# Performance work log

Measured on AMD Instinct MI355X. Metric: run time of the kernel, lower is better.

## Reference

```python
import jax, jax.numpy as jnp
import numpy as np
import math

BATCH, CLS, ATT_DIM, IMG_DIM = 256, 500, 1024, 1024
ATT_HC, HIDDEN_C = 256, 1024
T_TEMP = 10.0
DEGREE = 30
THRESH = math.cos(math.pi * DEGREE / 180.0)
NEG = -9.0e15


def setup_inputs() -> dict:
    key = jax.random.key(0)
    ks = jax.random.split(key, 9)
    inp = {
        "image_feats": jax.random.normal(ks[0], (BATCH, IMG_DIM), dtype=jnp.float32),
        "attributes": jax.random.normal(ks[1], (CLS, ATT_DIM), dtype=jnp.float32),
        "unused": 0,
        # learned parameters (kaiming-like scaling)
        "att_g": jax.random.normal(ks[2], (ATT_DIM, ATT_HC), dtype=jnp.float32) / math.sqrt(ATT_DIM),
        "img_w": jax.random.normal(ks[3], (IMG_DIM, HIDDEN_C), dtype=jnp.float32) / math.sqrt(IMG_DIM),
        "sem_w": jax.random.normal(ks[4], (ATT_DIM, HIDDEN_C), dtype=jnp.float32) / math.sqrt(ATT_DIM),
        "sem_b": jax.random.normal(ks[5], (1, HIDDEN_C), dtype=jnp.float32) / math.sqrt(IMG_DIM),
        "fc_w": jax.random.normal(ks[6], (1, HIDDEN_C), dtype=jnp.float32) / math.sqrt(HIDDEN_C),
        "fc_b": jax.random.normal(ks[7], (1,), dtype=jnp.float32) / math.sqrt(HIDDEN_C),
    }
    return inp


def _get_new_attribute(attributes, att_g):
    # project attributes, cosine similarity between all class pairs
    g = attributes @ att_g                                    # [cls, att_hC]
    gn = g / jnp.linalg.norm(g, axis=1, keepdims=True)        # row-normalize
    sim = gn @ gn.T                                           # [cls, cls] cosine sims
    raw = jnp.where(sim > THRESH, sim, NEG)                   # angular-threshold mask
    attention = jax.nn.softmax(raw * T_TEMP, axis=1)          # [cls, cls]
    return attention @ attributes                             # [cls, att_dim]


def reference(image_feats, attributes, unused, att_g, img_w, sem_w, sem_b, fc_w, fc_b):
    att_outs = _get_new_attribute(attributes, att_g)          # [cls, att_dim]
    # factor the broadcast: identical math to matmul on expanded tensors
    img_h = image_feats @ img_w                               # [batch, hidden]
    sem_h = att_outs @ sem_w                                  # [cls, hidden]
    hidden = jax.nn.relu(img_h[:, None, :] + sem_h[None, :, :] + sem_b[None, :, :])  # [batch, cls, hidden]
    out = jnp.einsum('bch,h->bc', hidden, fc_w[0]) + fc_b[0]  # [batch, cls]
    return out
```

## Files before the change

kernel.cpp:

```cpp
#include <hip/hip_runtime.h>
#include <math.h>

#define BATCH 256
#define CLS 500
#define T_TEMP_ 10.0f
#define THRESH_ 0.86602540378443864676f
#define NEGV -9.0e15f

typedef __attribute__((ext_vector_type(8))) short short8;
typedef __attribute__((ext_vector_type(8))) unsigned short u16x8;
typedef __attribute__((ext_vector_type(4))) unsigned short u16x4;
typedef __attribute__((ext_vector_type(4))) float f32x4;
typedef __attribute__((ext_vector_type(2))) float f32x2;

static __device__ __forceinline__ unsigned short f2bf(float x) {
    unsigned int u = __builtin_bit_cast(unsigned int, x);
    u += 0x7fff + ((u >> 16) & 1);
    return (unsigned short)(u >> 16);
}
static __device__ __forceinline__ float bf2f(unsigned short v) {
    return __builtin_bit_cast(float, (unsigned int)v << 16);
}
static __device__ __forceinline__ float fel(const float4& v, int j) { return (&v.x)[j]; }
static __device__ __forceinline__ u16x8 pack8(const float4& a, const float4& b) {
    u16x8 o;
    o[0] = f2bf(a.x); o[1] = f2bf(a.y); o[2] = f2bf(a.z); o[3] = f2bf(a.w);
    o[4] = f2bf(b.x); o[5] = f2bf(b.y); o[6] = f2bf(b.z); o[7] = f2bf(b.w);
    return o;
}

__global__ __launch_bounds__(256) void mega_gemm(
    const float* __restrict__ attrs, const float* __restrict__ attg,
    const float* __restrict__ imgf, const float* __restrict__ imgw,
    const float* __restrict__ semw,
    float* __restrict__ gpart, unsigned short* __restrict__ imgP,
    unsigned short* __restrict__ asemP)
{
    __shared__ unsigned short As[64][40];
    __shared__ unsigned short Bs[128][40];
    const int t = threadIdx.x;
    const int bid = blockIdx.x;

    const int w = t >> 6, lane = t & 63;
    const int wr = w >> 1, wc = w & 1;
    const int fr = lane & 15, kg = lane >> 4;
    const int as_row = t >> 2, as_kq = t & 3;
    const int bs_nc = (t & 31) * 4, bs_kr = t >> 5;

    const float* A; const float* Bf;
    int ar0, alim, n0, k0, klen, bstride, split;
    if (bid < 128) {
        const int mt = bid >> 4, nt = (bid >> 3) & 1; split = bid & 7;
        A = attrs; alim = CLS; ar0 = mt * 64;
        Bf = attg; bstride = 256; n0 = nt * 128;
        k0 = split * 128; klen = 128;
    } else if (bid < 192) {
        const int idx = bid - 128; split = idx & 1;
        const int nt = (idx >> 1) & 7, mt = idx >> 4;
        A = imgf; alim = 256; ar0 = mt * 64;
        Bf = imgw; bstride = 1024; n0 = nt * 128;
        k0 = split * 512; klen = 512;
    } else {
        const int idx = bid - 192; split = idx & 1;
        const int nt = (idx >> 1) & 7, mt = idx >> 4;
        A = attrs; alim = CLS; ar0 = mt * 64;
        Bf = semw; bstride = 1024; n0 = nt * 128;
        k0 = split * 512; klen = 512;
    }

    f32x4 acc[2][4];
    #pragma unroll
    for (int i = 0; i < 2; ++i)
        #pragma unroll
        for (int j = 0; j < 4; ++j) acc[i][j] = (f32x4){0.f, 0.f, 0.f, 0.f};

    for (int kb = k0; kb < k0 + klen; kb += 32) {
        {
            const int gr = ar0 + as_row;
            float4 v0 = make_float4(0.f,0.f,0.f,0.f), v1 = v0;
            if (gr < alim) {
                const float* ap = &A[(size_t)gr * 1024 + kb + as_kq * 8];
                v0 = *(const float4*)ap; v1 = *(const float4*)(ap + 4);
            }
            *(u16x8*)&As[as_row][as_kq * 8] = pack8(v0, v1);
        }
        {
            const float* bp = &Bf[(size_t)(kb + bs_kr * 4) * bstride + n0 + bs_nc];
            float4 r0 = *(const float4*)(bp);
            float4 r1 = *(const float4*)(bp + bstride);
            float4 r2 = *(const float4*)(bp + 2 * bstride);
            float4 r3 = *(const float4*)(bp + 3 * bstride);
            #pragma unroll
            for (int j = 0; j < 4; ++j) {
                unsigned int lo = (unsigned int)f2bf(fel(r0, j)) | ((unsigned int)f2bf(fel(r1, j)) << 16);
                unsigned int hi = (unsigned int)f2bf(fel(r2, j)) | ((unsigned int)f2bf(fel(r3, j)) << 16);
                uint2 u2; u2.x = lo; u2.y = hi;
                *(uint2*)&Bs[bs_nc + j][bs_kr * 4] = u2;
            }
        }
        __syncthreads();
        short8 af[2], bfr[4];
        #pragma unroll
        for (int i = 0; i < 2; ++i) af[i] = *(short8*)&As[wr * 32 + i * 16 + fr][kg * 8];
        #pragma unroll
        for (int j = 0; j < 4; ++j) bfr[j] = *(short8*)&Bs[wc * 64 + j * 16 + fr][kg * 8];
        #pragma unroll
        for (int i = 0; i < 2; ++i)
            #pragma unroll
            for (int j = 0; j < 4; ++j)
                acc[i][j] = __builtin_amdgcn_mfma_f32_16x16x32_bf16(af[i], bfr[j], acc[i][j], 0, 0, 0);
        __syncthreads();
    }

    const int orow0 = ar0 + wr * 32, ocol0 = n0 + wc * 64;
    if (bid < 128) {
        float* Gp = gpart + (size_t)split * (512 * 256);
        #pragma unroll
        for (int i = 0; i < 2; ++i) {
            const int r0 = orow0 + i * 16 + kg * 4;
            #pragma unroll
            for (int j = 0; j < 4; ++j) {
                const int cc = ocol0 + j * 16 + fr;
                #pragma unroll
                for (int r = 0; r < 4; ++r)
                    Gp[(size_t)(r0 + r) * 256 + cc] = acc[i][j][r];
            }
        }
    } else {
        unsigned short* Cw = (bid < 192)
            ? imgP  + (size_t)split * (256 * 1024)
            : asemP + (size_t)split * (512 * 1024);
        #pragma unroll
        for (int i = 0; i < 2; ++i) {
            const int r0 = orow0 + i * 16 + kg * 4;
            #pragma unroll
            for (int j = 0; j < 4; ++j) {
                const int cc = ocol0 + j * 16 + fr;
                #pragma unroll
                for (int r = 0; r < 4; ++r)
                    Cw[(size_t)(r0 + r) * 1024 + cc] = f2bf(acc[i][j][r]);
            }
        }
    }
}

__global__ __launch_bounds__(256) void reduce_norm_kernel(
    const float* __restrict__ part, unsigned short* __restrict__ gn_bf)
{
    const int c = blockIdx.x, t = threadIdx.x;
    float v = 0.f;
    #pragma unroll
    for (int z = 0; z < 8; ++z) v += part[(size_t)z * (512 * 256) + c * 256 + t];
    float ss = v * v;
    #pragma unroll
    for (int off = 32; off >= 1; off >>= 1) ss += __shfl_down(ss, off);
    __shared__ float red[4];
    const int wave = t >> 6, lane = t & 63;
    if (lane == 0) red[wave] = ss;
    __syncthreads();
    const float tot = red[0] + red[1] + red[2] + red[3];
    const float rn  = 1.f / sqrtf(tot);
    gn_bf[c * 256 + t] = f2bf(v * rn);
}

__global__ __launch_bounds__(256) void sim_kernel(
    const unsigned short* __restrict__ gn, float* __restrict__ S)
{
    __shared__ unsigned short As[64][40];
    __shared__ unsigned short Bs[128][40];
    const int t  = threadIdx.x;
    const int ar0 = blockIdx.x * 64;
    const int n0  = blockIdx.y * 128;

    const int w = t >> 6, lane = t & 63;
    const int wr = w >> 1, wc = w & 1;
    const int fr = lane & 15, kg = lane >> 4;
    const int a_row = t >> 2, a_k = (t & 3) * 8;
    const int b_row = t >> 1, b_k = (t & 1) * 16;
    const int gra = ar0 + a_row;
    const int grb = n0 + b_row;
    const bool va = gra < CLS;
    const bool vb = grb < CLS;
    const size_t abase = (size_t)gra * 256 + a_k;
    const size_t bbase = (size_t)grb * 256 + b_k;

    u16x8 zz = {0,0,0,0,0,0,0,0};
    u16x8 pa = zz, pb0 = zz, pb1 = zz;
    if (va) pa = *(const u16x8*)&gn[abase];
    if (vb) { pb0 = *(const u16x8*)&gn[bbase]; pb1 = *(const u16x8*)&gn[bbase + 8]; }

    f32x4 acc[2][4];
    #pragma unroll
    for (int i = 0; i < 2; ++i)
        #pragma unroll
        for (int j = 0; j < 4; ++j) acc[i][j] = (f32x4){0.f, 0.f, 0.f, 0.f};

    for (int kb = 0; kb < 256; kb += 32) {
        *(u16x8*)&As[a_row][a_k] = pa;
        *(u16x8*)&Bs[b_row][b_k] = pb0;
        *(u16x8*)&Bs[b_row][b_k + 8] = pb1;
        __syncthreads();

        const int kn = kb + 32;
        if (kn < 256) {
            if (va) pa = *(const u16x8*)&gn[abase + kn];
            if (vb) { pb0 = *(const u16x8*)&gn[bbase + kn]; pb1 = *(const u16x8*)&gn[bbase + kn + 8]; }
        }

        short8 af[2], bfr[4];
        #pragma unroll
        for (int i = 0; i < 2; ++i) af[i] = *(short8*)&As[wr * 32 + i * 16 + fr][kg * 8];
        #pragma unroll
        for (int j = 0; j < 4; ++j) bfr[j] = *(short8*)&Bs[wc * 64 + j * 16 + fr][kg * 8];
        #pragma unroll
        for (int i = 0; i < 2; ++i)
            #pragma unroll
            for (int j = 0; j < 4; ++j)
                acc[i][j] = __builtin_amdgcn_mfma_f32_16x16x32_bf16(af[i], bfr[j], acc[i][j], 0, 0, 0);
        __syncthreads();
    }

    const int orow0 = ar0 + wr * 32, ocol0 = n0 + wc * 64;
    #pragma unroll
    for (int i = 0; i < 2; ++i) {
        const int r0 = orow0 + i * 16 + kg * 4;
        #pragma unroll
        for (int j = 0; j < 4; ++j) {
            const int cc = ocol0 + j * 16 + fr;
            if (cc >= CLS) continue;
            #pragma unroll
            for (int r = 0; r < 4; ++r) {
                const int rr = r0 + r;
                if (rr < CLS) S[(size_t)rr * CLS + cc] = acc[i][j][r];
            }
        }
    }
}

__global__ __launch_bounds__(256) void softmax_gather_kernel(
    const float* __restrict__ sim, const unsigned short* __restrict__ asemP,
    const float* __restrict__ semb, unsigned short* __restrict__ sem_h)
{
    const int c = blockIdx.x, t = threadIdx.x;
    __shared__ float p_s[512];
    __shared__ float redm[4];
    __shared__ float reds[4];

    const float d0 = sim[(size_t)c * CLS + t];
    const float d1 = (t + 256 < CLS) ? sim[(size_t)c * CLS + t + 256] : NEGV;

    float vmax = fmaxf((d0 > THRESH_) ? d0 : NEGV, (d1 > THRESH_) ? d1 : NEGV);
    #pragma unroll
    for (int off = 32; off >= 1; off >>= 1) vmax = fmaxf(vmax, __shfl_down(vmax, off));
    const int wave = t >> 6, lane = t & 63;
    if (lane == 0) redm[wave] = vmax;
    __syncthreads();
    const float m = fmaxf(fmaxf(redm[0], redm[1]), fmaxf(redm[2], redm[3]));

    const float p0 = (d0 > THRESH_) ? expf(T_TEMP_ * (d0 - m)) : 0.f;
    const float p1 = (d1 > THRESH_) ? expf(T_TEMP_ * (d1 - m)) : 0.f;
    p_s[t] = p0;
    p_s[t + 256] = p1;
    float vsum = p0 + p1;
    #pragma unroll
    for (int off = 32; off >= 1; off >>= 1) vsum += __shfl_down(vsum, off);
    if (lane == 0) reds[wave] = vsum;
    __syncthreads();
    const float inv = 1.f / (reds[0] + reds[1] + reds[2] + reds[3]);

    float acc[4] = {0.f, 0.f, 0.f, 0.f};
    for (int base = 0; base < 512; base += 64) {
        const float pv_l = p_s[base + lane];
        unsigned long long mask = __ballot(pv_l > 0.f);
        while (mask) {
            const int l = __ffsll((long long)mask) - 1;
            mask &= mask - 1;
            const int c2 = base + l;
            const float pv = p_s[c2];
            const unsigned short* a0 = &asemP[(size_t)c2 * 1024 + t];
            const unsigned short* a1 = a0 + (size_t)512 * 1024;
            #pragma unroll
            for (int j = 0; j < 4; ++j)
                acc[j] += pv * (bf2f(a0[256 * j]) + bf2f(a1[256 * j]));
        }
    }
    #pragma unroll
    for (int j = 0; j < 4; ++j)
        sem_h[(size_t)c * 1024 + t + 256 * j] =
            f2bf(acc[j] * inv + semb[t + 256 * j]);
}

__global__ __launch_bounds__(256) void fused_out_partial(
    const unsigned short* __restrict__ imgP, const unsigned short* __restrict__ sem_h,
    const float* __restrict__ fc_w, float* __restrict__ outpart)
{
    __shared__ float imgs[64][36];
    __shared__ float sems[64][36];
    __shared__ float fcs[32];

    const size_t istride = (size_t)256 * 1024;
    const int t  = threadIdx.x;
    const int tb = t >> 4, tc = t & 15;
    const int b0 = blockIdx.x * 64, c0 = blockIdx.y * 64;
    const int h0 = blockIdx.z * 32;

    if (t < 8) *(float4*)&fcs[t * 4] = *(const float4*)&fc_w[h0 + t * 4];

    {
        const int row = t >> 2, col = (t & 3) * 8;
        f32x4 iv0 = {0.f,0.f,0.f,0.f}, iv1 = iv0;
        const unsigned short* pi = &imgP[(size_t)(b0 + row) * 1024 + h0 + col];
        #pragma unroll
        for (int z = 0; z < 2; ++z) {
            u16x8 vz = *(const u16x8*)(pi + (size_t)z * istride);
            iv0[0] += bf2f(vz[0]); iv0[1] += bf2f(vz[1]);
            iv0[2] += bf2f(vz[2]); iv0[3] += bf2f(vz[3]);
            iv1[0] += bf2f(vz[4]); iv1[1] += bf2f(vz[5]);
            iv1[2] += bf2f(vz[6]); iv1[3] += bf2f(vz[7]);
        }
        *(f32x4*)&imgs[row][col]     = iv0;
        *(f32x4*)&imgs[row][col + 4] = iv1;

        f32x4 sv0 = {0.f,0.f,0.f,0.f}, sv1 = sv0;
        if (c0 + row < CLS) {
            u16x8 vz = *(const u16x8*)&sem_h[(size_t)(c0 + row) * 1024 + h0 + col];
            sv0[0] = bf2f(vz[0]); sv0[1] = bf2f(vz[1]);
            sv0[2] = bf2f(vz[2]); sv0[3] = bf2f(vz[3]);
            sv1[0] = bf2f(vz[4]); sv1[1] = bf2f(vz[5]);
            sv1[2] = bf2f(vz[6]); sv1[3] = bf2f(vz[7]);
        }
        *(f32x4*)&sems[row][col]     = sv0;
        *(f32x4*)&sems[row][col + 4] = sv1;
    }
    __syncthreads();

    f32x2 acc2[4][4];
    #pragma unroll
    for (int i = 0; i < 4; ++i)
        #pragma unroll
        for (int j = 0; j < 4; ++j) acc2[i][j] = (f32x2){0.f, 0.f};

    #pragma unroll
    for (int h4 = 0; h4 < 8; ++h4) {
        f32x4 ia[4], sa[4];
        #pragma unroll
        for (int i = 0; i < 4; ++i) ia[i] = *(f32x4*)&imgs[tb + 16 * i][h4 * 4];
        #pragma unroll
        for (int j = 0; j < 4; ++j) sa[j] = *(f32x4*)&sems[tc + 16 * j][h4 * 4];
        const f32x4 wv = *(const f32x4*)&fcs[h4 * 4];
        #pragma unroll
        for (int e2 = 0; e2 < 2; ++e2) {
            const f32x2 w2 = {wv[2 * e2], wv[2 * e2 + 1]};
            f32x2 ia2[4], sa2[4];
            #pragma unroll
            for (int i = 0; i < 4; ++i) ia2[i] = (f32x2){ia[i][2 * e2], ia[i][2 * e2 + 1]};
            #pragma unroll
            for (int j = 0; j < 4; ++j) sa2[j] = (f32x2){sa[j][2 * e2], sa[j][2 * e2 + 1]};
            #pragma unroll
            for (int i = 0; i < 4; ++i)
                #pragma unroll
                for (int j = 0; j < 4; ++j) {
                    f32x2 s = ia2[i] + sa2[j];
                    s = __builtin_elementwise_max(s, (f32x2){0.f, 0.f});
                    acc2[i][j] += s * w2;
                }
        }
    }

    const int nh = blockIdx.z;
    #pragma unroll
    for (int i = 0; i < 4; ++i) {
        const int b = b0 + tb + 16 * i;
        #pragma unroll
        for (int j = 0; j < 4; ++j) {
            const int cc = c0 + tc + 16 * j;
            if (cc < CLS)
                outpart[((size_t)nh * BATCH + b) * CLS + cc] = acc2[i][j][0] + acc2[i][j][1];
        }
    }
}

__global__ __launch_bounds__(256) void finalize_kernel(
    const float* __restrict__ partial, const float* __restrict__ fc_b,
    float* __restrict__ out)
{
    const int idx = blockIdx.x * 256 + threadIdx.x;
    if (idx >= BATCH * CLS) return;
    float s = fc_b[0];
    #pragma unroll
    for (int nh = 0; nh < 32; ++nh)
        s += partial[(size_t)nh * (BATCH * CLS) + idx];
    out[idx] = s;
}

extern "C" void kernel_launch(void* const* d_in, const int* in_sizes, int n_in,
                              void* d_out, int out_size, void* d_ws, size_t ws_size,
                              hipStream_t stream)
{
    const float* imgf  = (const float*)d_in[0];
    const float* attrs = (const float*)d_in[1];
    const float* attg  = (const float*)d_in[3];
    const float* imgw  = (const float*)d_in[4];
    const float* semw  = (const float*)d_in[5];
    const float* semb  = (const float*)d_in[6];
    const float* fcw   = (const float*)d_in[7];
    const float* fcb   = (const float*)d_in[8];
    float* out = (float*)d_out;

    char* ws = (char*)d_ws;
    size_t off = 0;
    auto alloc = [&](size_t b) { size_t o = off; off = (off + b + 255) & ~(size_t)255; return o; };
    float* gpart          = (float*)(ws + alloc((size_t)8 * 512 * 256 * 4));
    unsigned short* gn_bf = (unsigned short*)(ws + alloc((size_t)500 * 256 * 2));
    float* sim            = (float*)(ws + alloc((size_t)CLS * CLS * 4));
    unsigned short* imgP  = (unsigned short*)(ws + alloc((size_t)2 * 256 * 1024 * 2));
    unsigned short* asemP = (unsigned short*)(ws + alloc((size_t)2 * 512 * 1024 * 2));
    unsigned short* sem_h = (unsigned short*)(ws + alloc((size_t)500 * 1024 * 2));
    float* outP           = (float*)(ws + alloc((size_t)32 * BATCH * CLS * 4));

    mega_gemm<<<320, 256, 0, stream>>>(attrs, attg, imgf, imgw, semw,
                                       gpart, imgP, asemP);
    reduce_norm_kernel<<<CLS, 256, 0, stream>>>(gpart, gn_bf);
    sim_kernel<<<dim3(8, 4), 256, 0, stream>>>(gn_bf, sim);
    softmax_gather_kernel<<<CLS, 256, 0, stream>>>(sim, asemP, semb, sem_h);
    fused_out_partial<<<dim3(4, 8, 32), 256, 0, stream>>>(imgP, sem_h, fcw, outP);
    finalize_kernel<<<(BATCH * CLS + 255) / 256, 256, 0, stream>>>(outP, fcb, out);
}
```

Before: 64.44 us.

## Fuse similarity GEMM with softmax and sparse gather into one kernel

Merges the cosine-similarity GEMM and the softmax/gather kernels into a single kernel. Each of 8 blocks computes a 64-row strip of the similarity matrix into LDS, then computes a thresholded softmax per row and records up to 16 nonzero weights with their column indices. It then gathers the weighted attribute projections, falling back to a full scan when a row has more than 16 hits. This removes the global round trip of the similarity matrix and one kernel launch. The cost is that only 8 blocks run, and each block walks its 64 rows one after another, so parallelism is far lower than the previous 500-block gather. The kernel also needs roughly 150 KB of LDS per block.

```diff
diff --git a/kernel.cpp b/kernel.cpp
--- a/kernel.cpp
+++ b/kernel.cpp
@@ -6,6 +6,7 @@
 #define T_TEMP_ 10.0f
 #define THRESH_ 0.86602540378443864676f
 #define NEGV -9.0e15f
+#define CAP 16
 
 typedef __attribute__((ext_vector_type(8))) short short8;
 typedef __attribute__((ext_vector_type(8))) unsigned short u16x8;
@@ -163,131 +164,172 @@
     gn_bf[c * 256 + t] = f2bf(v * rn);
 }
 
-__global__ __launch_bounds__(256) void sim_kernel(
-    const unsigned short* __restrict__ gn, float* __restrict__ S)
-{
+__global__ __launch_bounds__(256) void sim_softmax_gather(
+    const unsigned short* __restrict__ gn, const unsigned short* __restrict__ asemP,
+    const float* __restrict__ semb, unsigned short* __restrict__ sem_h)
+{
+    __shared__ float simS[64][512];
     __shared__ unsigned short As[64][40];
     __shared__ unsigned short Bs[128][40];
-    const int t  = threadIdx.x;
-    const int ar0 = blockIdx.x * 64;
-    const int n0  = blockIdx.y * 128;
-
+    __shared__ int   cnt_s[64];
+    __shared__ int   hitc2[64][CAP];
+    __shared__ float hitw[64][CAP];
+    __shared__ float mrow[64];
+    __shared__ float invrow[64];
+
+    const int t = threadIdx.x;
+    const int r0g = blockIdx.x * 64;
     const int w = t >> 6, lane = t & 63;
     const int wr = w >> 1, wc = w & 1;
     const int fr = lane & 15, kg = lane >> 4;
     const int a_row = t >> 2, a_k = (t & 3) * 8;
     const int b_row = t >> 1, b_k = (t & 1) * 16;
-    const int gra = ar0 + a_row;
-    const int grb = n0 + b_row;
+
+    const int gra = r0g + a_row;
     const bool va = gra < CLS;
-    const bool vb = grb < CLS;
     const size_t abase = (size_t)gra * 256 + a_k;
-    const size_t bbase = (size_t)grb * 256 + b_k;
-
-    u16x8 zz = {0,0,0,0,0,0,0,0};
-    u16x8 pa = zz, pb0 = zz, pb1 = zz;
-    if (va) pa = *(const u16x8*)&gn[abase];
-    if (vb) { pb0 = *(const u16x8*)&gn[bbase]; pb1 = *(const u16x8*)&gn[bbase + 8]; }
-
-    f32x4 acc[2][4];
-    #pragma unroll
-    for (int i = 0; i < 2; ++i)
-        #pragma unroll
-        for (int j = 0; j < 4; ++j) acc[i][j] = (f32x4){0.f, 0.f, 0.f, 0.f};
-
-    for (int kb = 0; kb < 256; kb += 32) {
-        *(u16x8*)&As[a_row][a_k] = pa;
-        *(u16x8*)&Bs[b_row][b_k] = pb0;
-        *(u16x8*)&Bs[b_row][b_k + 8] = pb1;
-        __syncthreads();
-
-        const int kn = kb + 32;
-        if (kn < 256) {
-            if (va) pa = *(const u16x8*)&gn[abase + kn];
-            if (vb) { pb0 = *(const u16x8*)&gn[bbase + kn]; pb1 = *(const u16x8*)&gn[bbase + kn + 8]; }
-        }
-
-        short8 af[2], bfr[4];
-        #pragma unroll
-        for (int i = 0; i < 2; ++i) af[i] = *(short8*)&As[wr * 32 + i * 16 + fr][kg * 8];
-        #pragma unroll
-        for (int j = 0; j < 4; ++j) bfr[j] = *(short8*)&Bs[wc * 64 + j * 16 + fr][kg * 8];
+
+    for (int nt = 0; nt < 4; ++nt) {
+        const int n0 = nt * 128;
+        const int grb = n0 + b_row;
+        const bool vb = grb < CLS;
+        const size_t bbase = (size_t)grb * 256 + b_k;
+
+        u16x8 zz = {0,0,0,0,0,0,0,0};
+        u16x8 pa = zz, pb0 = zz, pb1 = zz;
+        if (va) pa = *(const u16x8*)&gn[abase];
+        if (vb) { pb0 = *(const u16x8*)&gn[bbase]; pb1 = *(const u16x8*)&gn[bbase + 8]; }
+
+        f32x4 acc[2][4];
         #pragma unroll
         for (int i = 0; i < 2; ++i)
             #pragma unroll
-            for (int j = 0; j < 4; ++j)
-                acc[i][j] = __builtin_amdgcn_mfma_f32_16x16x32_bf16(af[i], bfr[j], acc[i][j], 0, 0, 0);
-        __syncthreads();
-    }
-
-    const int orow0 = ar0 + wr * 32, ocol0 = n0 + wc * 64;
-    #pragma unroll
-    for (int i = 0; i < 2; ++i) {
-        const int r0 = orow0 + i * 16 + kg * 4;
-        #pragma unroll
-        for (int j = 0; j < 4; ++j) {
-            const int cc = ocol0 + j * 16 + fr;
-            if (cc >= CLS) continue;
-            #pragma unroll
-            for (int r = 0; r < 4; ++r) {
-                const int rr = r0 + r;
-                if (rr < CLS) S[(size_t)rr * CLS + cc] = acc[i][j][r];
-            }
-        }
-    }
-}
-
-__global__ __launch_bounds__(256) void softmax_gather_kernel(
-    const float* __restrict__ sim, const unsigned short* __restrict__ asemP,
-    const float* __restrict__ semb, unsigned short* __restrict__ sem_h)
-{
-    const int c = blockIdx.x, t = threadIdx.x;
-    __shared__ float p_s[512];
-    __shared__ float redm[4];
-    __shared__ float reds[4];
-
-    const float d0 = sim[(size_t)c * CLS + t];
-    const float d1 = (t + 256 < CLS) ? sim[(size_t)c * CLS + t + 256] : NEGV;
-
-    float vmax = fmaxf((d0 > THRESH_) ? d0 : NEGV, (d1 > THRESH_) ? d1 : NEGV);
-    #pragma unroll
-    for (int off = 32; off >= 1; off >>= 1) vmax = fmaxf(vmax, __shfl_down(vmax, off));
-    const int wave = t >> 6, lane = t & 63;
-    if (lane == 0) redm[wave] = vmax;
+            for (int j = 0; j < 4; ++j) acc[i][j] = (f32x4){0.f, 0.f, 0.f, 0.f};
+
+        for (int kb = 0; kb < 256; kb += 32) {
+            *(u16x8*)&As[a_row][a_k] = pa;
+            *(u16x8*)&Bs[b_row][b_k] = pb0;
+            *(u16x8*)&Bs[b_row][b_k + 8] = pb1;
+            __syncthreads();
+
+            const int kn = kb + 32;
+            if (kn < 256) {
+                if (va) pa = *(const u16x8*)&gn[abase + kn];
+                if (vb) { pb0 = *(const u16x8*)&gn[bbase + kn]; pb1 = *(const u16x8*)&gn[bbase + kn + 8]; }
+            }
+
+            short8 af[2], bfr[4];
+            #pragma unroll
+            for (int i = 0; i < 2; ++i) af[i] = *(short8*)&As[wr * 32 + i * 16 + fr][kg * 8];
+            #pragma unroll
+            for (int j = 0; j < 4; ++j) bfr[j] = *(short8*)&Bs[wc * 64 + j * 16 + fr][kg * 8];
+            #pragma unroll
+            for (int i = 0; i < 2; ++i)
+                #pragma unroll
+                for (int j = 0; j < 4; ++j)
+                    acc[i][j] = __builtin_amdgcn_mfma_f32_16x16x32_bf16(af[i], bfr[j], acc[i][j], 0, 0, 0);
+            __syncthreads();
+        }
+
+        const int orow0 = wr * 32, ocol0 = n0 + wc * 64;
+        #pragma unroll
+        for (int i = 0; i < 2; ++i) {
+            const int r0 = orow0 + i * 16 + kg * 4;
+            #pragma unroll
+            for (int j = 0; j < 4; ++j) {
+                const int cc = ocol0 + j * 16 + fr;
+                #pragma unroll
+                for (int r = 0; r < 4; ++r)
+                    simS[r0 + r][cc] = acc[i][j][r];
+            }
+        }
+    }
     __syncthreads();
-    const float m = fmaxf(fmaxf(redm[0], redm[1]), fmaxf(redm[2], redm[3]));
-
-    const float p0 = (d0 > THRESH_) ? expf(T_TEMP_ * (d0 - m)) : 0.f;
-    const float p1 = (d1 > THRESH_) ? expf(T_TEMP_ * (d1 - m)) : 0.f;
-    p_s[t] = p0;
-    p_s[t + 256] = p1;
-    float vsum = p0 + p1;
-    #pragma unroll
-    for (int off = 32; off >= 1; off >>= 1) vsum += __shfl_down(vsum, off);
-    if (lane == 0) reds[wave] = vsum;
+
+    for (int i = 0; i < 16; ++i) {
+        const int rl = w * 16 + i;
+        const int r  = r0g + rl;
+        float vals[8];
+        float vmax = NEGV;
+        if (r < CLS) {
+            #pragma unroll
+            for (int ch = 0; ch < 8; ++ch) {
+                const int c2 = ch * 64 + lane;
+                const float d = (c2 < CLS) ? simS[rl][c2] : NEGV;
+                vals[ch] = d;
+                vmax = fmaxf(vmax, (d > THRESH_) ? d : NEGV);
+            }
+        } else {
+            #pragma unroll
+            for (int ch = 0; ch < 8; ++ch) vals[ch] = NEGV;
+        }
+        #pragma unroll
+        for (int off = 32; off >= 1; off >>= 1) vmax = fmaxf(vmax, __shfl_down(vmax, off));
+        vmax = __shfl(vmax, 0);
+        float pvs[8];
+        float s = 0.f;
+        #pragma unroll
+        for (int ch = 0; ch < 8; ++ch) {
+            const float pv = (vals[ch] > THRESH_) ? expf(T_TEMP_ * (vals[ch] - vmax)) : 0.f;
+            pvs[ch] = pv; s += pv;
+        }
+        #pragma unroll
+        for (int off = 32; off >= 1; off >>= 1) s += __shfl_down(s, off);
+        s = __shfl(s, 0);
+        const float inv = (r < CLS) ? 1.f / s : 0.f;
+        int count = 0;
+        #pragma unroll
+        for (int ch = 0; ch < 8; ++ch) {
+            unsigned long long mk = __ballot(pvs[ch] > 0.f);
+            while (mk) {
+                const int l = __ffsll((long long)mk) - 1;
+                mk &= mk - 1;
+                const float wgt = __shfl(pvs[ch], l) * inv;
+                if (count < CAP && lane == 0) {
+                    hitc2[rl][count] = ch * 64 + l;
+                    hitw[rl][count]  = wgt;
+                }
+                ++count;
+            }
+        }
+        if (lane == 0) { cnt_s[rl] = count; mrow[rl] = vmax; invrow[rl] = inv; }
+    }
     __syncthreads();
-    const float inv = 1.f / (reds[0] + reds[1] + reds[2] + reds[3]);
-
-    float acc[4] = {0.f, 0.f, 0.f, 0.f};
-    for (int base = 0; base < 512; base += 64) {
-        const float pv_l = p_s[base + lane];
-        unsigned long long mask = __ballot(pv_l > 0.f);
-        while (mask) {
-            const int l = __ffsll((long long)mask) - 1;
-            mask &= mask - 1;
-            const int c2 = base + l;
-            const float pv = p_s[c2];
-            const unsigned short* a0 = &asemP[(size_t)c2 * 1024 + t];
-            const unsigned short* a1 = a0 + (size_t)512 * 1024;
-            #pragma unroll
-            for (int j = 0; j < 4; ++j)
-                acc[j] += pv * (bf2f(a0[256 * j]) + bf2f(a1[256 * j]));
-        }
-    }
-    #pragma unroll
-    for (int j = 0; j < 4; ++j)
-        sem_h[(size_t)c * 1024 + t + 256 * j] =
-            f2bf(acc[j] * inv + semb[t + 256 * j]);
+
+    for (int rl = 0; rl < 64; ++rl) {
+        const int r = r0g + rl;
+        if (r >= CLS) continue;
+        float acc[4] = {0.f, 0.f, 0.f, 0.f};
+        const int n = cnt_s[rl];
+        if (n <= CAP) {
+            for (int k = 0; k < n; ++k) {
+                const int c2 = hitc2[rl][k];
+                const float wgt = hitw[rl][k];
+                const unsigned short* a0 = &asemP[(size_t)c2 * 1024 + t];
+                const unsigned short* a1 = a0 + (size_t)512 * 1024;
+                #pragma unroll
+                for (int j = 0; j < 4; ++j)
+                    acc[j] += wgt * (bf2f(a0[256 * j]) + bf2f(a1[256 * j]));
+            }
+        } else {
+            const float mr = mrow[rl], ir = invrow[rl];
+            for (int c2 = 0; c2 < CLS; ++c2) {
+                const float d = simS[rl][c2];
+                if (d > THRESH_) {
+                    const float wgt = expf(T_TEMP_ * (d - mr)) * ir;
+                    const unsigned short* a0 = &asemP[(size_t)c2 * 1024 + t];
+                    const unsigned short* a1 = a0 + (size_t)512 * 1024;
+                    #pragma unroll
+                    for (int j = 0; j < 4; ++j)
+                        acc[j] += wgt * (bf2f(a0[256 * j]) + bf2f(a1[256 * j]));
+                }
+            }
+        }
+        #pragma unroll
+        for (int j = 0; j < 4; ++j)
+            sem_h[(size_t)r * 1024 + t + 256 * j] =
+                f2bf(acc[j] + semb[t + 256 * j]);
+    }
 }
 
 __global__ __launch_bounds__(256) void fused_out_partial(
@@ -412,7 +454,6 @@
     auto alloc = [&](size_t b) { size_t o = off; off = (off + b + 255) & ~(size_t)255; return o; };
     float* gpart          = (float*)(ws + alloc((size_t)8 * 512 * 256 * 4));
     unsigned short* gn_bf = (unsigned short*)(ws + alloc((size_t)500 * 256 * 2));
-    float* sim            = (float*)(ws + alloc((size_t)CLS * CLS * 4));
     unsigned short* imgP  = (unsigned short*)(ws + alloc((size_t)2 * 256 * 1024 * 2));
     unsigned short* asemP = (unsigned short*)(ws + alloc((size_t)2 * 512 * 1024 * 2));
     unsigned short* sem_h = (unsigned short*)(ws + alloc((size_t)500 * 1024 * 2));
@@ -421,8 +462,7 @@
     mega_gemm<<<320, 256, 0, stream>>>(attrs, attg, imgf, imgw, semw,
                                        gpart, imgP, asemP);
     reduce_norm_kernel<<<CLS, 256, 0, stream>>>(gpart, gn_bf);
-    sim_kernel<<<dim3(8, 4), 256, 0, stream>>>(gn_bf, sim);
-    softmax_gather_kernel<<<CLS, 256, 0, stream>>>(sim, asemP, semb, sem_h);
+    sim_softmax_gather<<<8, 256, 0, stream>>>(gn_bf, asemP, semb, sem_h);
     fused_out_partial<<<dim3(4, 8, 32), 256, 0, stream>>>(imgP, sem_h, fcw, outP);
     finalize_kernel<<<(BATCH * CLS + 255) / 256, 256, 0, stream>>>(outP, fcb, out);
 }
```

Result: slower. 126.5 us (+96.3%).

## Fuse softmax-gather with output reduction per class; drop split-K in projection GEMMs

Applied to the files above, without the earlier changes.

Removes split-K for the image and semantic projection GEMMs so each block covers the full K range and writes a single bf16 result. The softmax-gather kernel now keeps sem_h in shared memory and computes the whole hidden-dim relu-dot for all 256 batch rows of its class, so the 32-way partial output buffer and the finalize kernel go away. This cuts launches and a large partial write and read, at the cost of fewer GEMM blocks (less parallelism). Each class block also restreams the full imgH (512 KB) through shared memory, and the final output stores are strided by class.

```diff
diff --git a/kernel.cpp b/kernel.cpp
--- a/kernel.cpp
+++ b/kernel.cpp
@@ -11,7 +11,6 @@
 typedef __attribute__((ext_vector_type(8))) unsigned short u16x8;
 typedef __attribute__((ext_vector_type(4))) unsigned short u16x4;
 typedef __attribute__((ext_vector_type(4))) float f32x4;
-typedef __attribute__((ext_vector_type(2))) float f32x2;
 
 static __device__ __forceinline__ unsigned short f2bf(float x) {
     unsigned int u = __builtin_bit_cast(unsigned int, x);
@@ -33,8 +32,8 @@
     const float* __restrict__ attrs, const float* __restrict__ attg,
     const float* __restrict__ imgf, const float* __restrict__ imgw,
     const float* __restrict__ semw,
-    float* __restrict__ gpart, unsigned short* __restrict__ imgP,
-    unsigned short* __restrict__ asemP)
+    float* __restrict__ gpart, unsigned short* __restrict__ imgH,
+    unsigned short* __restrict__ asem)
 {
     __shared__ unsigned short As[64][40];
     __shared__ unsigned short Bs[128][40];
@@ -48,24 +47,24 @@
     const int bs_nc = (t & 31) * 4, bs_kr = t >> 5;
 
     const float* A; const float* Bf;
-    int ar0, alim, n0, k0, klen, bstride, split;
+    int ar0, alim, n0, k0, klen, bstride, split = 0;
     if (bid < 128) {
         const int mt = bid >> 4, nt = (bid >> 3) & 1; split = bid & 7;
         A = attrs; alim = CLS; ar0 = mt * 64;
         Bf = attg; bstride = 256; n0 = nt * 128;
         k0 = split * 128; klen = 128;
-    } else if (bid < 192) {
-        const int idx = bid - 128; split = idx & 1;
-        const int nt = (idx >> 1) & 7, mt = idx >> 4;
+    } else if (bid < 160) {
+        const int idx = bid - 128;
+        const int mt = idx >> 3, nt = idx & 7;
         A = imgf; alim = 256; ar0 = mt * 64;
         Bf = imgw; bstride = 1024; n0 = nt * 128;
-        k0 = split * 512; klen = 512;
+        k0 = 0; klen = 1024;
     } else {
-        const int idx = bid - 192; split = idx & 1;
-        const int nt = (idx >> 1) & 7, mt = idx >> 4;
+        const int idx = bid - 160;
+        const int mt = idx >> 3, nt = idx & 7;
         A = attrs; alim = CLS; ar0 = mt * 64;
         Bf = semw; bstride = 1024; n0 = nt * 128;
-        k0 = split * 512; klen = 512;
+        k0 = 0; klen = 1024;
     }
 
     f32x4 acc[2][4];
@@ -127,9 +126,7 @@
             }
         }
     } else {
-        unsigned short* Cw = (bid < 192)
-            ? imgP  + (size_t)split * (256 * 1024)
-            : asemP + (size_t)split * (512 * 1024);
+        unsigned short* Cw = (bid < 160) ? imgH : asem;
         #pragma unroll
         for (int i = 0; i < 2; ++i) {
             const int r0 = orow0 + i * 16 + kg * 4;
@@ -237,14 +234,20 @@
     }
 }
 
-__global__ __launch_bounds__(256) void softmax_gather_kernel(
-    const float* __restrict__ sim, const unsigned short* __restrict__ asemP,
-    const float* __restrict__ semb, unsigned short* __restrict__ sem_h)
-{
-    const int c = blockIdx.x, t = threadIdx.x;
+__global__ __launch_bounds__(256) void colout_kernel(
+    const float* __restrict__ sim, const unsigned short* __restrict__ asem,
+    const unsigned short* __restrict__ imgH, const float* __restrict__ semb,
+    const float* __restrict__ fcw, const float* __restrict__ fcb,
+    float* __restrict__ out)
+{
     __shared__ float p_s[512];
     __shared__ float redm[4];
     __shared__ float reds[4];
+    __shared__ float sems[1024];
+    __shared__ float imgs[256][67];
+
+    const int c = blockIdx.x, t = threadIdx.x;
+    const int wave = t >> 6, lane = t & 63;
 
     const float d0 = sim[(size_t)c * CLS + t];
     const float d1 = (t + 256 < CLS) ? sim[(size_t)c * CLS + t + 256] : NEGV;
@@ -252,7 +255,6 @@
     float vmax = fmaxf((d0 > THRESH_) ? d0 : NEGV, (d1 > THRESH_) ? d1 : NEGV);
     #pragma unroll
     for (int off = 32; off >= 1; off >>= 1) vmax = fmaxf(vmax, __shfl_down(vmax, off));
-    const int wave = t >> 6, lane = t & 63;
     if (lane == 0) redm[wave] = vmax;
     __syncthreads();
     const float m = fmaxf(fmaxf(redm[0], redm[1]), fmaxf(redm[2], redm[3]));
@@ -277,120 +279,37 @@
             mask &= mask - 1;
             const int c2 = base + l;
             const float pv = p_s[c2];
-            const unsigned short* a0 = &asemP[(size_t)c2 * 1024 + t];
-            const unsigned short* a1 = a0 + (size_t)512 * 1024;
-            #pragma unroll
-            for (int j = 0; j < 4; ++j)
-                acc[j] += pv * (bf2f(a0[256 * j]) + bf2f(a1[256 * j]));
+            const unsigned short* ar = &asem[(size_t)c2 * 1024 + t];
+            #pragma unroll
+            for (int j = 0; j < 4; ++j) acc[j] += pv * bf2f(ar[256 * j]);
         }
     }
     #pragma unroll
     for (int j = 0; j < 4; ++j)
-        sem_h[(size_t)c * 1024 + t + 256 * j] =
-            f2bf(acc[j] * inv + semb[t + 256 * j]);
-}
-
-__global__ __launch_bounds__(256) void fused_out_partial(
-    const unsigned short* __restrict__ imgP, const unsigned short* __restrict__ sem_h,
-    const float* __restrict__ fc_w, float* __restrict__ outpart)
-{
-    __shared__ float imgs[64][36];
-    __shared__ float sems[64][36];
-    __shared__ float fcs[32];
-
-    const size_t istride = (size_t)256 * 1024;
-    const int t  = threadIdx.x;
-    const int tb = t >> 4, tc = t & 15;
-    const int b0 = blockIdx.x * 64, c0 = blockIdx.y * 64;
-    const int h0 = blockIdx.z * 32;
-
-    if (t < 8) *(float4*)&fcs[t * 4] = *(const float4*)&fc_w[h0 + t * 4];
-
-    {
-        const int row = t >> 2, col = (t & 3) * 8;
-        f32x4 iv0 = {0.f,0.f,0.f,0.f}, iv1 = iv0;
-        const unsigned short* pi = &imgP[(size_t)(b0 + row) * 1024 + h0 + col];
-        #pragma unroll
-        for (int z = 0; z < 2; ++z) {
-            u16x8 vz = *(const u16x8*)(pi + (size_t)z * istride);
-            iv0[0] += bf2f(vz[0]); iv0[1] += bf2f(vz[1]);
-            iv0[2] += bf2f(vz[2]); iv0[3] += bf2f(vz[3]);
-            iv1[0] += bf2f(vz[4]); iv1[1] += bf2f(vz[5]);
-            iv1[2] += bf2f(vz[6]); iv1[3] += bf2f(vz[7]);
-        }
-        *(f32x4*)&imgs[row][col]     = iv0;
-        *(f32x4*)&imgs[row][col + 4] = iv1;
-
-        f32x4 sv0 = {0.f,0.f,0.f,0.f}, sv1 = sv0;
-        if (c0 + row < CLS) {
-            u16x8 vz = *(const u16x8*)&sem_h[(size_t)(c0 + row) * 1024 + h0 + col];
-            sv0[0] = bf2f(vz[0]); sv0[1] = bf2f(vz[1]);
-            sv0[2] = bf2f(vz[2]); sv0[3] = bf2f(vz[3]);
-            sv1[0] = bf2f(vz[4]); sv1[1] = bf2f(vz[5]);
-            sv1[2] = bf2f(vz[6]); sv1[3] = bf2f(vz[7]);
-        }
-        *(f32x4*)&sems[row][col]     = sv0;
-        *(f32x4*)&sems[row][col + 4] = sv1;
-    }
+        sems[t + 256 * j] = acc[j] * inv + semb[t + 256 * j];
     __syncthreads();
 
-    f32x2 acc2[4][4];
-    #pragma unroll
-    for (int i = 0; i < 4; ++i)
-        #pragma unroll
-        for (int j = 0; j < 4; ++j) acc2[i][j] = (f32x2){0.f, 0.f};
-
-    #pragma unroll
-    for (int h4 = 0; h4 < 8; ++h4) {
-        f32x4 ia[4], sa[4];
-        #pragma unroll
-        for (int i = 0; i < 4; ++i) ia[i] = *(f32x4*)&imgs[tb + 16 * i][h4 * 4];
-        #pragma unroll
-        for (int j = 0; j < 4; ++j) sa[j] = *(f32x4*)&sems[tc + 16 * j][h4 * 4];
-        const f32x4 wv = *(const f32x4*)&fcs[h4 * 4];
-        #pragma unroll
-        for (int e2 = 0; e2 < 2; ++e2) {
-            const f32x2 w2 = {wv[2 * e2], wv[2 * e2 + 1]};
-            f32x2 ia2[4], sa2[4];
-            #pragma unroll
-            for (int i = 0; i < 4; ++i) ia2[i] = (f32x2){ia[i][2 * e2], ia[i][2 * e2 + 1]};
-            #pragma unroll
-            for (int j = 0; j < 4; ++j) sa2[j] = (f32x2){sa[j][2 * e2], sa[j][2 * e2 + 1]};
-            #pragma unroll
-            for (int i = 0; i < 4; ++i)
-                #pragma unroll
-                for (int j = 0; j < 4; ++j) {
-                    f32x2 s = ia2[i] + sa2[j];
-                    s = __builtin_elementwise_max(s, (f32x2){0.f, 0.f});
-                    acc2[i][j] += s * w2;
-                }
-        }
-    }
-
-    const int nh = blockIdx.z;
-    #pragma unroll
-    for (int i = 0; i < 4; ++i) {
-        const int b = b0 + tb + 16 * i;
-        #pragma unroll
-        for (int j = 0; j < 4; ++j) {
-            const int cc = c0 + tc + 16 * j;
-            if (cc < CLS)
-                outpart[((size_t)nh * BATCH + b) * CLS + cc] = acc2[i][j][0] + acc2[i][j][1];
-        }
-    }
-}
-
-__global__ __launch_bounds__(256) void finalize_kernel(
-    const float* __restrict__ partial, const float* __restrict__ fc_b,
-    float* __restrict__ out)
-{
-    const int idx = blockIdx.x * 256 + threadIdx.x;
-    if (idx >= BATCH * CLS) return;
-    float s = fc_b[0];
-    #pragma unroll
-    for (int nh = 0; nh < 32; ++nh)
-        s += partial[(size_t)nh * (BATCH * CLS) + idx];
-    out[idx] = s;
+    float oacc = 0.f;
+    for (int hc = 0; hc < 16; ++hc) {
+        #pragma unroll
+        for (int it = 0; it < 16; ++it) {
+            const int row = it * 16 + (t >> 4);
+            const int col = (t & 15) * 4;
+            u16x4 v = *(const u16x4*)&imgH[(size_t)row * 1024 + hc * 64 + col];
+            imgs[row][col + 0] = bf2f(v[0]);
+            imgs[row][col + 1] = bf2f(v[1]);
+            imgs[row][col + 2] = bf2f(v[2]);
+            imgs[row][col + 3] = bf2f(v[3]);
+        }
+        __syncthreads();
+        const float* sp = &sems[hc * 64];
+        const float* fp = &fcw[hc * 64];
+        #pragma unroll
+        for (int h = 0; h < 64; ++h)
+            oacc += fmaxf(imgs[t][h] + sp[h], 0.f) * fp[h];
+        __syncthreads();
+    }
+    out[(size_t)t * CLS + c] = oacc + fcb[0];
 }
 
 extern "C" void kernel_launch(void* const* d_in, const int* in_sizes, int n_in,
@@ -413,16 +332,12 @@
     float* gpart          = (float*)(ws + alloc((size_t)8 * 512 * 256 * 4));
     unsigned short* gn_bf = (unsigned short*)(ws + alloc((size_t)500 * 256 * 2));
     float* sim            = (float*)(ws + alloc((size_t)CLS * CLS * 4));
-    unsigned short* imgP  = (unsigned short*)(ws + alloc((size_t)2 * 256 * 1024 * 2));
-    unsigned short* asemP = (unsigned short*)(ws + alloc((size_t)2 * 512 * 1024 * 2));
-    unsigned short* sem_h = (unsigned short*)(ws + alloc((size_t)500 * 1024 * 2));
-    float* outP           = (float*)(ws + alloc((size_t)32 * BATCH * CLS * 4));
-
-    mega_gemm<<<320, 256, 0, stream>>>(attrs, attg, imgf, imgw, semw,
-                                       gpart, imgP, asemP);
+    unsigned short* imgH  = (unsigned short*)(ws + alloc((size_t)256 * 1024 * 2));
+    unsigned short* asem  = (unsigned short*)(ws + alloc((size_t)512 * 1024 * 2));
+
+    mega_gemm<<<224, 256, 0, stream>>>(attrs, attg, imgf, imgw, semw,
+                                       gpart, imgH, asem);
     reduce_norm_kernel<<<CLS, 256, 0, stream>>>(gpart, gn_bf);
     sim_kernel<<<dim3(8, 4), 256, 0, stream>>>(gn_bf, sim);
-    softmax_gather_kernel<<<CLS, 256, 0, stream>>>(sim, asemP, semb, sem_h);
-    fused_out_partial<<<dim3(4, 8, 32), 256, 0, stream>>>(imgP, sem_h, fcw, outP);
-    finalize_kernel<<<(BATCH * CLS + 255) / 256, 256, 0, stream>>>(outP, fcb, out);
-}
+    colout_kernel<<<CLS, 256, 0, stream>>>(sim, asem, imgH, semb, fcw, fcb, out);
+}
```

Result: slower. 87.48 us (+35.7%).
